# Performance work log

Measured on AMD Instinct MI355X. Metric: run time of the kernel, lower is better.

## Reference

```python
import jax, jax.numpy as jnp
import numpy as np

S, I, M = 8, 64, 256  # streams, modulations per stream, features per stream
N = 16384             # batch


def setup_inputs() -> dict:
    key = jax.random.key(0)
    ks = jax.random.split(key, 11)
    sc_x = 1.0 / np.sqrt(I)
    sc_h = 1.0 / np.sqrt(2 * M)
    return {
        "modulation": jax.random.normal(ks[0], (N, S * I), jnp.float32),
        "h0": jnp.zeros((1, S * M), jnp.float32),
        "c0": jnp.zeros((1, S * M), jnp.float32),
        "Wx": jax.random.normal(ks[1], (S, M, I), jnp.float32) * sc_x,
        "bx": jax.random.normal(ks[2], (S, M), jnp.float32) * 0.01,
        "Wi": jax.random.normal(ks[3], (S, M, 2 * M), jnp.float32) * sc_h,
        "bi": jax.random.normal(ks[4], (S, M), jnp.float32) * 0.01,
        "Wf": jax.random.normal(ks[5], (S, M, 2 * M), jnp.float32) * sc_h,
        "bf": jax.random.normal(ks[6], (S, M), jnp.float32) * 0.01,
        "Wg": jax.random.normal(ks[7], (S, M, 2 * M), jnp.float32) * sc_h,
        "bg": jax.random.normal(ks[8], (S, M), jnp.float32) * 0.01,
        "Wo": jax.random.normal(ks[9], (S, M, 2 * M), jnp.float32) * sc_h,
        "bo": jax.random.normal(ks[10], (S, M), jnp.float32) * 0.01,
    }


def reference(modulation, h0, c0, Wx, bx, Wi, bi, Wf, bf, Wg, bg, Wo, bo):
    n = modulation.shape[0]
    # grouped (per-stream) linear: [N,S,I] x [S,M,I] -> [N,S,M]
    m = modulation.reshape(n, S, I)
    x = jnp.einsum('nsi,smi->nsm', m, Wx) + bx  # nonlinear=None -> identity, gamma=1; dropout p=0 -> identity
    h_prev = jnp.broadcast_to(h0.reshape(1, S, M), (n, S, M))
    c_prev = c0.reshape(1, S, M)
    # cat_groups: per-stream concat of [x_s, h_s] -> [N,S,2M]
    xh = jnp.concatenate([x, h_prev], axis=-1)
    i = jax.nn.sigmoid(jnp.einsum('nsk,smk->nsm', xh, Wi) + bi)
    f = jax.nn.sigmoid(jnp.einsum('nsk,smk->nsm', xh, Wf) + bf)
    g = jnp.tanh(jnp.einsum('nsk,smk->nsm', xh, Wg) + bg)
    o = jax.nn.sigmoid(jnp.einsum('nsk,smk->nsm', xh, Wo) + bo)
    c = f * c_prev + i * g
    h = o * jnp.tanh(c)
    return h.reshape(n, S * M)
```

## Files before the change

### kernel.cpp

```cpp
#include <hip/hip_runtime.h>
#include <hip/hip_bf16.h>

using bf16 = __hip_bfloat16;
typedef __attribute__((ext_vector_type(8))) short bf16x8;
typedef __attribute__((ext_vector_type(4))) float f32x4;

constexpr int S = 8, I = 64, M = 256, N = 16384;
constexpr int SM = S * M;
constexpr int MODROW = S * I;
constexpr int OUTROW = S * M;
constexpr int TILES = 8;

__device__ __forceinline__ short f2bf_s(float f) {
    union { bf16 b; short s; } u; u.b = __float2bfloat16(f); return u.s;
}
__device__ __forceinline__ bf16x8 cvt8(const float* p) {
    const float4 x = ((const float4*)p)[0];
    const float4 y = ((const float4*)p)[1];
    bf16x8 r;
    r[0] = f2bf_s(x.x); r[1] = f2bf_s(x.y); r[2] = f2bf_s(x.z); r[3] = f2bf_s(x.w);
    r[4] = f2bf_s(y.x); r[5] = f2bf_s(y.y); r[6] = f2bf_s(y.z); r[7] = f2bf_s(y.w);
    return r;
}

__device__ __forceinline__ float sigmoid_f(float x) {
    return __builtin_amdgcn_rcpf(1.f + __expf(-x));
}
__device__ __forceinline__ float tanh_f(float x) {
    return 2.f * __builtin_amdgcn_rcpf(1.f + __expf(-2.f * x)) - 1.f;
}

__global__ __launch_bounds__(256) void cvt_mod(
    const float* __restrict__ in, bf16* __restrict__ outb)
{
    const size_t i = ((size_t)blockIdx.x * 256 + threadIdx.x) * 8;
    *(bf16x8*)(outb + i) = cvt8(in + i);
}

__global__ __launch_bounds__(64) void precompute_kernel(
    const float* __restrict__ Wx, const float* __restrict__ bx,
    const float* __restrict__ Wi, const float* __restrict__ bi,
    const float* __restrict__ Wf, const float* __restrict__ bfv,
    const float* __restrict__ Wg, const float* __restrict__ bg,
    const float* __restrict__ Wo, const float* __restrict__ bo,
    const float* __restrict__ h0,
    bf16* __restrict__ Weff, float* __restrict__ beff)
{
    const int blk = blockIdx.x;
    const int mc  = blk & 63;
    const int g   = (blk >> 6) & 3;
    const int s   = blk >> 8;
    const int k   = threadIdx.x;

    const float* WG = (g == 0) ? Wi : (g == 1) ? Wf : (g == 2) ? Wg : Wo;
    const float* bG = (g == 0) ? bi : (g == 1) ? bfv : (g == 2) ? bg : bo;

    const int sm0 = s * 256 + mc * 4;
    const float* w0 = WG + (size_t)(sm0 + 0) * 512;
    const float* w1 = WG + (size_t)(sm0 + 1) * 512;
    const float* w2 = WG + (size_t)(sm0 + 2) * 512;
    const float* w3 = WG + (size_t)(sm0 + 3) * 512;
    const float* wxs = Wx + (size_t)s * (256 * 64) + k;

    float a0 = 0.f, a1 = 0.f, a2 = 0.f, a3 = 0.f;
    for (int j = 0; j < 256; j += 8) {
#pragma unroll
        for (int u = 0; u < 8; ++u) {
            const float wx = wxs[(size_t)(j + u) * 64];
            a0 = fmaf(w0[j + u], wx, a0);
            a1 = fmaf(w1[j + u], wx, a1);
            a2 = fmaf(w2[j + u], wx, a2);
            a3 = fmaf(w3[j + u], wx, a3);
        }
    }
    Weff[((size_t)(sm0 + 0) * 4 + g) * 64 + k] = __float2bfloat16(a0);
    Weff[((size_t)(sm0 + 1) * 4 + g) * 64 + k] = __float2bfloat16(a1);
    Weff[((size_t)(sm0 + 2) * 4 + g) * 64 + k] = __float2bfloat16(a2);
    Weff[((size_t)(sm0 + 3) * 4 + g) * 64 + k] = __float2bfloat16(a3);

    float b0 = 0.f, b1 = 0.f, b2 = 0.f, b3 = 0.f;
#pragma unroll
    for (int t = 0; t < 4; ++t) {
        const int j = k + t * 64;
        const float xb = bx[(s << 8) + j];
        const float xh = h0[(s << 8) + j];
        b0 = fmaf(w0[j], xb, b0); b0 = fmaf(w0[256 + j], xh, b0);
        b1 = fmaf(w1[j], xb, b1); b1 = fmaf(w1[256 + j], xh, b1);
        b2 = fmaf(w2[j], xb, b2); b2 = fmaf(w2[256 + j], xh, b2);
        b3 = fmaf(w3[j], xb, b3); b3 = fmaf(w3[256 + j], xh, b3);
    }
#pragma unroll
    for (int off = 32; off > 0; off >>= 1) {
        b0 += __shfl_down(b0, off);
        b1 += __shfl_down(b1, off);
        b2 += __shfl_down(b2, off);
        b3 += __shfl_down(b3, off);
    }
    if (k == 0) {
        beff[g * SM + sm0 + 0] = b0 + bG[sm0 + 0];
        beff[g * SM + sm0 + 1] = b1 + bG[sm0 + 1];
        beff[g * SM + sm0 + 2] = b2 + bG[sm0 + 2];
        beff[g * SM + sm0 + 3] = b3 + bG[sm0 + 3];
    }
}

__global__ __launch_bounds__(256) void lstm_main_bf(
    const bf16* __restrict__ modb, const float* __restrict__ c0,
    const bf16* __restrict__ Weff, const float* __restrict__ beff,
    float* __restrict__ out)
{
    const int wave = threadIdx.x >> 6;
    const int lane = threadIdx.x & 63;
    const int quad = lane >> 4;
    const int col  = lane & 15;

    const int s  = blockIdx.y >> 2;
    const int mq = blockIdx.y & 3;
    const int m0 = mq * 64 + wave * 16;
    const int sm_tile = s * 256 + m0;

    const bf16* abase = Weff + ((size_t)(sm_tile + col) * 4) * 64 + quad * 8;
    bf16x8 afrag[4][2];
#pragma unroll
    for (int g = 0; g < 4; ++g) {
        afrag[g][0] = *(const bf16x8*)(abase + (size_t)g * 64);
        afrag[g][1] = *(const bf16x8*)(abase + (size_t)g * 64 + 32);
    }

    const int sm4 = sm_tile + quad * 4;
    const f32x4 c0v = *(const f32x4*)(c0 + sm4);
    f32x4 bias[4];
#pragma unroll
    for (int g = 0; g < 4; ++g)
        bias[g] = *(const f32x4*)(beff + g * SM + sm4);

    const int nbase = blockIdx.x * (16 * TILES);
    const bf16* brow0 = modb + (size_t)(nbase + col) * MODROW + s * I + quad * 8;

    bf16x8 b0 = *(const bf16x8*)(brow0);
    bf16x8 b1 = *(const bf16x8*)(brow0 + 32);

#pragma unroll
    for (int t = 0; t < TILES; ++t) {
        bf16x8 nb0, nb1;
        if (t + 1 < TILES) {
            const bf16* brow = brow0 + (size_t)(t + 1) * 16 * MODROW;
            nb0 = *(const bf16x8*)(brow);
            nb1 = *(const bf16x8*)(brow + 32);
        }

        f32x4 acc[4];
#pragma unroll
        for (int g = 0; g < 4; ++g) {
            f32x4 c = bias[g];
            c = __builtin_amdgcn_mfma_f32_16x16x32_bf16(afrag[g][0], b0, c, 0, 0, 0);
            c = __builtin_amdgcn_mfma_f32_16x16x32_bf16(afrag[g][1], b1, c, 0, 0, 0);
            acc[g] = c;
        }

        const int n = nbase + t * 16 + col;
        f32x4 hv;
#pragma unroll
        for (int r = 0; r < 4; ++r) {
            const float iv = sigmoid_f(acc[0][r]);
            const float fv = sigmoid_f(acc[1][r]);
            const float gv = tanh_f(acc[2][r]);
            const float ov = sigmoid_f(acc[3][r]);
            const float cc = fv * c0v[r] + iv * gv;
            hv[r] = ov * tanh_f(cc);
        }
        *(f32x4*)(out + (size_t)n * OUTROW + sm4) = hv;

        if (t + 1 < TILES) { b0 = nb0; b1 = nb1; }
    }
}

__global__ __launch_bounds__(256) void lstm_main_f32(
    const float* __restrict__ mod, const float* __restrict__ c0,
    const bf16* __restrict__ Weff, const float* __restrict__ beff,
    float* __restrict__ out)
{
    const int wave = threadIdx.x >> 6;
    const int lane = threadIdx.x & 63;
    const int quad = lane >> 4;
    const int col  = lane & 15;

    const int s  = blockIdx.y >> 2;
    const int mq = blockIdx.y & 3;
    const int m0 = mq * 64 + wave * 16;
    const int sm_tile = s * 256 + m0;

    const bf16* abase = Weff + ((size_t)(sm_tile + col) * 4) * 64 + quad * 8;
    bf16x8 afrag[4][2];
#pragma unroll
    for (int g = 0; g < 4; ++g) {
        afrag[g][0] = *(const bf16x8*)(abase + (size_t)g * 64);
        afrag[g][1] = *(const bf16x8*)(abase + (size_t)g * 64 + 32);
    }

    const int sm4 = sm_tile + quad * 4;
    const f32x4 c0v = *(const f32x4*)(c0 + sm4);
    f32x4 bias[4];
#pragma unroll
    for (int g = 0; g < 4; ++g)
        bias[g] = *(const f32x4*)(beff + g * SM + sm4);

    const int nbase = blockIdx.x * (16 * TILES);
    const float* brow0 = mod + (size_t)(nbase + col) * MODROW + s * I + quad * 8;

    bf16x8 b0 = cvt8(brow0);
    bf16x8 b1 = cvt8(brow0 + 32);

#pragma unroll
    for (int t = 0; t < TILES; ++t) {
        bf16x8 nb0, nb1;
        if (t + 1 < TILES) {
            const float* brow = brow0 + (size_t)(t + 1) * 16 * MODROW;
            nb0 = cvt8(brow);
            nb1 = cvt8(brow + 32);
        }
        f32x4 acc[4];
#pragma unroll
        for (int g = 0; g < 4; ++g) {
            f32x4 c = bias[g];
            c = __builtin_amdgcn_mfma_f32_16x16x32_bf16(afrag[g][0], b0, c, 0, 0, 0);
            c = __builtin_amdgcn_mfma_f32_16x16x32_bf16(afrag[g][1], b1, c, 0, 0, 0);
            acc[g] = c;
        }
        const int n = nbase + t * 16 + col;
        f32x4 hv;
#pragma unroll
        for (int r = 0; r < 4; ++r) {
            const float iv = sigmoid_f(acc[0][r]);
            const float fv = sigmoid_f(acc[1][r]);
            const float gv = tanh_f(acc[2][r]);
            const float ov = sigmoid_f(acc[3][r]);
            const float cc = fv * c0v[r] + iv * gv;
            hv[r] = ov * tanh_f(cc);
        }
        *(f32x4*)(out + (size_t)n * OUTROW + sm4) = hv;
        if (t + 1 < TILES) { b0 = nb0; b1 = nb1; }
    }
}

extern "C" void kernel_launch(void* const* d_in, const int* in_sizes, int n_in,
                              void* d_out, int out_size, void* d_ws, size_t ws_size,
                              hipStream_t stream) {
    const float* mod = (const float*)d_in[0];
    const float* h0  = (const float*)d_in[1];
    const float* c0  = (const float*)d_in[2];
    const float* Wx  = (const float*)d_in[3];
    const float* bx  = (const float*)d_in[4];
    const float* Wi  = (const float*)d_in[5];
    const float* bi  = (const float*)d_in[6];
    const float* Wf  = (const float*)d_in[7];
    const float* bfv = (const float*)d_in[8];
    const float* Wg  = (const float*)d_in[9];
    const float* bg  = (const float*)d_in[10];
    const float* Wo  = (const float*)d_in[11];
    const float* bo  = (const float*)d_in[12];
    float* out = (float*)d_out;

    const size_t weff_b = (size_t)SM * 4 * 64 * sizeof(bf16);
    const size_t beff_b = (size_t)4 * SM * sizeof(float);
    const size_t modb_b = (size_t)N * MODROW * sizeof(bf16);
    bf16*  Weff = (bf16*)d_ws;
    float* beff = (float*)((char*)d_ws + weff_b);
    bf16*  modb = (bf16*)((char*)d_ws + weff_b + beff_b);

    precompute_kernel<<<2048, 64, 0, stream>>>(Wx, bx, Wi, bi, Wf, bfv,
                                               Wg, bg, Wo, bo, h0, Weff, beff);

    if (ws_size >= weff_b + beff_b + modb_b) {
        cvt_mod<<<(N * MODROW) / (8 * 256), 256, 0, stream>>>(mod, modb);
        lstm_main_bf<<<dim3(N / (16 * TILES), S * 4), 256, 0, stream>>>(
            modb, c0, Weff, beff, out);
    } else {
        lstm_main_f32<<<dim3(N / (16 * TILES), S * 4), 256, 0, stream>>>(
            mod, c0, Weff, beff, out);
    }
}
```

Measured before the change: 256.0 us.

## Fuse weight precompute with bf16 input conversion and fold exp2 scaling into weights

Merges the weight-precompute and modulation-to-bf16 conversion into one launch, and repacks the precompute so each 256-thread block handles four units with one wave each. The -log2e and -2log2e factors are folded into the effective weights and biases, so the gates can use exp2 directly instead of scaling before exp. The output store and the input loads in the conversion path become nontemporal. This saves a kernel launch and some per-element multiplies, but the pre-scaled values are rounded to bf16, which changes numerics slightly.

```diff
diff --git a/kernel.cpp b/kernel.cpp
--- a/kernel.cpp
+++ b/kernel.cpp
@@ -11,33 +11,38 @@
 constexpr int OUTROW = S * M;
 constexpr int TILES = 8;
 
+constexpr float LOG2E = 1.4426950408889634f;
+constexpr float KSIG  = -LOG2E;
+constexpr float KTANH = -2.0f * LOG2E;
+
 __device__ __forceinline__ short f2bf_s(float f) {
     union { bf16 b; short s; } u; u.b = __float2bfloat16(f); return u.s;
 }
 __device__ __forceinline__ bf16x8 cvt8(const float* p) {
-    const float4 x = ((const float4*)p)[0];
-    const float4 y = ((const float4*)p)[1];
+    const f32x4 x = ((const f32x4*)p)[0];
+    const f32x4 y = ((const f32x4*)p)[1];
     bf16x8 r;
-    r[0] = f2bf_s(x.x); r[1] = f2bf_s(x.y); r[2] = f2bf_s(x.z); r[3] = f2bf_s(x.w);
-    r[4] = f2bf_s(y.x); r[5] = f2bf_s(y.y); r[6] = f2bf_s(y.z); r[7] = f2bf_s(y.w);
+    r[0] = f2bf_s(x[0]); r[1] = f2bf_s(x[1]); r[2] = f2bf_s(x[2]); r[3] = f2bf_s(x[3]);
+    r[4] = f2bf_s(y[0]); r[5] = f2bf_s(y[1]); r[6] = f2bf_s(y[2]); r[7] = f2bf_s(y[3]);
     return r;
 }
 
-__device__ __forceinline__ float sigmoid_f(float x) {
-    return __builtin_amdgcn_rcpf(1.f + __expf(-x));
-}
-__device__ __forceinline__ float tanh_f(float x) {
-    return 2.f * __builtin_amdgcn_rcpf(1.f + __expf(-2.f * x)) - 1.f;
-}
-
-__global__ __launch_bounds__(256) void cvt_mod(
-    const float* __restrict__ in, bf16* __restrict__ outb)
-{
-    const size_t i = ((size_t)blockIdx.x * 256 + threadIdx.x) * 8;
-    *(bf16x8*)(outb + i) = cvt8(in + i);
-}
-
-__global__ __launch_bounds__(64) void precompute_kernel(
+__device__ __forceinline__ float exp2_f(float x) {
+#if __has_builtin(__builtin_amdgcn_exp2f)
+    return __builtin_amdgcn_exp2f(x);
+#else
+    return __expf(x * 0.6931471805599453f);
+#endif
+}
+__device__ __forceinline__ float rcp_f(float x) { return __builtin_amdgcn_rcpf(x); }
+__device__ __forceinline__ float sig2_f(float y)  { return rcp_f(1.f + exp2_f(y)); }
+__device__ __forceinline__ float tanh2_f(float y) { return fmaf(2.f, rcp_f(1.f + exp2_f(y)), -1.f); }
+
+constexpr int PRE_BLOCKS = 512;
+constexpr int CVT_BLOCKS = (N * MODROW) / (8 * 256);
+
+__global__ __launch_bounds__(256) void prep_fused(
+    const float* __restrict__ mod, bf16* __restrict__ modb,
     const float* __restrict__ Wx, const float* __restrict__ bx,
     const float* __restrict__ Wi, const float* __restrict__ bi,
     const float* __restrict__ Wf, const float* __restrict__ bfv,
@@ -46,14 +51,28 @@
     const float* __restrict__ h0,
     bf16* __restrict__ Weff, float* __restrict__ beff)
 {
-    const int blk = blockIdx.x;
-    const int mc  = blk & 63;
-    const int g   = (blk >> 6) & 3;
-    const int s   = blk >> 8;
-    const int k   = threadIdx.x;
+    if (blockIdx.x >= PRE_BLOCKS) {
+        const size_t i =
+            ((size_t)(blockIdx.x - PRE_BLOCKS) * 256 + threadIdx.x) * 8;
+        const f32x4 x = __builtin_nontemporal_load((const f32x4*)(mod + i));
+        const f32x4 y = __builtin_nontemporal_load((const f32x4*)(mod + i) + 1);
+        bf16x8 r;
+        r[0] = f2bf_s(x[0]); r[1] = f2bf_s(x[1]); r[2] = f2bf_s(x[2]); r[3] = f2bf_s(x[3]);
+        r[4] = f2bf_s(y[0]); r[5] = f2bf_s(y[1]); r[6] = f2bf_s(y[2]); r[7] = f2bf_s(y[3]);
+        *(bf16x8*)(modb + i) = r;
+        return;
+    }
+
+    const int unit = __builtin_amdgcn_readfirstlane(
+        blockIdx.x * 4 + (threadIdx.x >> 6));
+    const int k  = threadIdx.x & 63;
+    const int mc = unit & 63;
+    const int g  = (unit >> 6) & 3;
+    const int s  = unit >> 8;
 
     const float* WG = (g == 0) ? Wi : (g == 1) ? Wf : (g == 2) ? Wg : Wo;
     const float* bG = (g == 0) ? bi : (g == 1) ? bfv : (g == 2) ? bg : bo;
+    const float  kg = (g == 2) ? KTANH : KSIG;
 
     const int sm0 = s * 256 + mc * 4;
     const float* w0 = WG + (size_t)(sm0 + 0) * 512;
@@ -73,10 +92,10 @@
             a3 = fmaf(w3[j + u], wx, a3);
         }
     }
-    Weff[((size_t)(sm0 + 0) * 4 + g) * 64 + k] = __float2bfloat16(a0);
-    Weff[((size_t)(sm0 + 1) * 4 + g) * 64 + k] = __float2bfloat16(a1);
-    Weff[((size_t)(sm0 + 2) * 4 + g) * 64 + k] = __float2bfloat16(a2);
-    Weff[((size_t)(sm0 + 3) * 4 + g) * 64 + k] = __float2bfloat16(a3);
+    Weff[((size_t)(sm0 + 0) * 4 + g) * 64 + k] = __float2bfloat16(a0 * kg);
+    Weff[((size_t)(sm0 + 1) * 4 + g) * 64 + k] = __float2bfloat16(a1 * kg);
+    Weff[((size_t)(sm0 + 2) * 4 + g) * 64 + k] = __float2bfloat16(a2 * kg);
+    Weff[((size_t)(sm0 + 3) * 4 + g) * 64 + k] = __float2bfloat16(a3 * kg);
 
     float b0 = 0.f, b1 = 0.f, b2 = 0.f, b3 = 0.f;
 #pragma unroll
@@ -97,10 +116,10 @@
         b3 += __shfl_down(b3, off);
     }
     if (k == 0) {
-        beff[g * SM + sm0 + 0] = b0 + bG[sm0 + 0];
-        beff[g * SM + sm0 + 1] = b1 + bG[sm0 + 1];
-        beff[g * SM + sm0 + 2] = b2 + bG[sm0 + 2];
-        beff[g * SM + sm0 + 3] = b3 + bG[sm0 + 3];
+        beff[g * SM + sm0 + 0] = (b0 + bG[sm0 + 0]) * kg;
+        beff[g * SM + sm0 + 1] = (b1 + bG[sm0 + 1]) * kg;
+        beff[g * SM + sm0 + 2] = (b2 + bG[sm0 + 2]) * kg;
+        beff[g * SM + sm0 + 3] = (b3 + bG[sm0 + 3]) * kg;
     }
 }
 
@@ -162,14 +181,14 @@
         f32x4 hv;
 #pragma unroll
         for (int r = 0; r < 4; ++r) {
-            const float iv = sigmoid_f(acc[0][r]);
-            const float fv = sigmoid_f(acc[1][r]);
-            const float gv = tanh_f(acc[2][r]);
-            const float ov = sigmoid_f(acc[3][r]);
-            const float cc = fv * c0v[r] + iv * gv;
-            hv[r] = ov * tanh_f(cc);
-        }
-        *(f32x4*)(out + (size_t)n * OUTROW + sm4) = hv;
+            const float iv = sig2_f(acc[0][r]);
+            const float fv = sig2_f(acc[1][r]);
+            const float gv = tanh2_f(acc[2][r]);
+            const float ov = sig2_f(acc[3][r]);
+            const float cc = fmaf(fv, c0v[r], iv * gv);
+            hv[r] = ov * tanh2_f(cc * KTANH);
+        }
+        __builtin_nontemporal_store(hv, (f32x4*)(out + (size_t)n * OUTROW + sm4));
 
         if (t + 1 < TILES) { b0 = nb0; b1 = nb1; }
     }
@@ -231,14 +250,14 @@
         f32x4 hv;
 #pragma unroll
         for (int r = 0; r < 4; ++r) {
-            const float iv = sigmoid_f(acc[0][r]);
-            const float fv = sigmoid_f(acc[1][r]);
-            const float gv = tanh_f(acc[2][r]);
-            const float ov = sigmoid_f(acc[3][r]);
-            const float cc = fv * c0v[r] + iv * gv;
-            hv[r] = ov * tanh_f(cc);
-        }
-        *(f32x4*)(out + (size_t)n * OUTROW + sm4) = hv;
+            const float iv = sig2_f(acc[0][r]);
+            const float fv = sig2_f(acc[1][r]);
+            const float gv = tanh2_f(acc[2][r]);
+            const float ov = sig2_f(acc[3][r]);
+            const float cc = fmaf(fv, c0v[r], iv * gv);
+            hv[r] = ov * tanh2_f(cc * KTANH);
+        }
+        __builtin_nontemporal_store(hv, (f32x4*)(out + (size_t)n * OUTROW + sm4));
         if (t + 1 < TILES) { b0 = nb0; b1 = nb1; }
     }
 }
@@ -268,14 +287,14 @@
     float* beff = (float*)((char*)d_ws + weff_b);
     bf16*  modb = (bf16*)((char*)d_ws + weff_b + beff_b);
 
-    precompute_kernel<<<2048, 64, 0, stream>>>(Wx, bx, Wi, bi, Wf, bfv,
-                                               Wg, bg, Wo, bo, h0, Weff, beff);
-
     if (ws_size >= weff_b + beff_b + modb_b) {
-        cvt_mod<<<(N * MODROW) / (8 * 256), 256, 0, stream>>>(mod, modb);
+        prep_fused<<<PRE_BLOCKS + CVT_BLOCKS, 256, 0, stream>>>(
+            mod, modb, Wx, bx, Wi, bi, Wf, bfv, Wg, bg, Wo, bo, h0, Weff, beff);
         lstm_main_bf<<<dim3(N / (16 * TILES), S * 4), 256, 0, stream>>>(
             modb, c0, Weff, beff, out);
     } else {
+        prep_fused<<<PRE_BLOCKS, 256, 0, stream>>>(
+            mod, modb, Wx, bx, Wi, bi, Wf, bfv, Wg, bg, Wo, bo, h0, Weff, beff);
         lstm_main_f32<<<dim3(N / (16 * TILES), S * 4), 256, 0, stream>>>(
             mod, c0, Weff, beff, out);
     }
```

Measured after the change: 250.9 us. 2.0% less time.
